# Performance work log

Hardware: AMD Instinct MI355X
Metric: run time of the kernel (lower is better)

## Reference

```python
import jax, jax.numpy as jnp
import numpy as np

T, H, E, I, K = 4096, 2048, 8, 1408, 2


def setup_inputs() -> dict:
    key = jax.random.key(0)
    k1, k2, k3, k4 = jax.random.split(key, 4)
    x = jax.random.normal(k1, (T, H), dtype=jnp.float32)
    router_w = jax.random.normal(k2, (H, E), dtype=jnp.float32) * 0.02
    gate_up_proj = jax.random.normal(k3, (E, H, 2 * I), dtype=jnp.float32) * 0.02
    down_proj = jax.random.normal(k4, (E, I, H), dtype=jnp.float32) * 0.02
    return {"x": x, "router_w": router_w, "gate_up_proj": gate_up_proj, "down_proj": down_proj}


def _moe_forward(x, router_w, gate_up_proj, down_proj):
    # --- Router: softmax over experts, top-k selection (Qwen2-MoE style) ---
    logits = x @ router_w                                  # [T, E]
    probs = jax.nn.softmax(logits, axis=-1)
    topk_w, topk_idx = jax.lax.top_k(probs, K)             # [T, K]

    # --- Permute: replicate tokens per selected expert, stable-sort by expert id ---
    flat_eid = topk_idx.reshape(-1)                        # [T*K]
    rep_x = jnp.repeat(x, K, axis=0)                       # [T*K, H]
    sort_idx = jnp.argsort(flat_eid, stable=True)          # token permute (like ops.permute)
    perm_x = rep_x[sort_idx]                               # [T*K, H] grouped by expert
    perm_eid = flat_eid[sort_idx]                          # [T*K]

    # --- Grouped expert MLP (gate_up GEMM -> SiLU*up -> down GEMM) ---
    # Faithful to grouped-GEMM math; expressed as a fixed loop over E experts
    # with row masking to stay jit-compatible (no data-dependent shapes).
    out = jnp.zeros_like(perm_x)
    for e in range(E):
        gu = perm_x @ gate_up_proj[e]                      # [T*K, 2I]
        gate, up = gu[:, :I], gu[:, I:]
        h = (jax.nn.silu(gate) * up) @ down_proj[e]        # [T*K, H]
        out = out + jnp.where((perm_eid == e)[:, None], h, 0.0)

    # --- Unpermute + weighted combine over top-k ---
    inv_sort = jnp.argsort(sort_idx)                       # inverse permute mapping
    unperm = out[inv_sort].reshape(T, K, H)
    return jnp.einsum('tkh,tk->th', unperm, topk_w)        # [T, H]


def reference(x, router_w, gate_up_proj, down_proj):
    return _moe_forward(x, router_w, gate_up_proj, down_proj)
```

## Files before the change

### kernel.cpp

```cpp
#include <hip/hip_runtime.h>
#include <hip/hip_bf16.h>

#define T_TOK 4096
#define H_DIM 2048
#define E_NUM 8
#define I_DIM 1408
#define RTOT  8192
#define MAXMT 40
#define NT1   11
#define NKT1  64
#define NT2   8
#define NKT2  44

#define QBLK  2080
#define AREG  8320
#define BUFU  16640
#define LDSZ  (4 * BUFU * 2)

typedef __bf16 bf16x8 __attribute__((ext_vector_type(8)));
typedef float  floatx4 __attribute__((ext_vector_type(4)));
typedef unsigned short ushortx8 __attribute__((ext_vector_type(8)));

#define VMCNT(n) asm volatile("s_waitcnt vmcnt(" #n ")" ::: "memory")

__device__ __forceinline__ unsigned short f2bf(float f) {
  union { float f; unsigned u; } v; v.f = f;
  unsigned r = v.u + 0x7FFFu + ((v.u >> 16) & 1u);
  return (unsigned short)(r >> 16);
}

__device__ __forceinline__ void async16(const void* g, void* l) {
  __builtin_amdgcn_global_load_lds(
      (__attribute__((address_space(1))) void*)(g),
      (__attribute__((address_space(3))) void*)(l), 16, 0, 0);
}

__global__ void router_kernel(const float* __restrict__ x, const float* __restrict__ rw,
                              int* __restrict__ topk_idx, float* __restrict__ topk_w,
                              int* __restrict__ counts) {
  int wave = threadIdx.x >> 6, lane = threadIdx.x & 63;
  int t = blockIdx.x * 4 + wave;
  const float* xr = x + (size_t)t * H_DIM;
  float acc[E_NUM];
#pragma unroll
  for (int e = 0; e < E_NUM; e++) acc[e] = 0.f;
  for (int h = lane; h < H_DIM; h += 64) {
    float xv = xr[h];
    const float* wr = rw + h * E_NUM;
#pragma unroll
    for (int e = 0; e < E_NUM; e++) acc[e] += xv * wr[e];
  }
#pragma unroll
  for (int e = 0; e < E_NUM; e++) {
    float v = acc[e];
#pragma unroll
    for (int s = 32; s > 0; s >>= 1) v += __shfl_xor(v, s, 64);
    acc[e] = v;
  }
  if (lane == 0) {
    float mx = acc[0];
#pragma unroll
    for (int e = 1; e < E_NUM; e++) mx = fmaxf(mx, acc[e]);
    float p[E_NUM], s = 0.f;
#pragma unroll
    for (int e = 0; e < E_NUM; e++) { p[e] = __expf(acc[e] - mx); s += p[e]; }
    float inv = 1.0f / s;
    int i0 = 0;
#pragma unroll
    for (int e = 1; e < E_NUM; e++) if (p[e] > p[i0]) i0 = e;
    int i1 = (i0 == 0) ? 1 : 0;
#pragma unroll
    for (int e = 0; e < E_NUM; e++) if (e != i0 && p[e] > p[i1]) i1 = e;
    topk_idx[t * 2]     = i0;
    topk_idx[t * 2 + 1] = i1;
    topk_w[t * 2]       = p[i0] * inv;
    topk_w[t * 2 + 1]   = p[i1] * inv;
    atomicAdd(&counts[i0], 1);
    atomicAdd(&counts[i1], 1);
  }
}

__global__ void scan_kernel(const int* __restrict__ counts, int* __restrict__ cursors,
                            int* __restrict__ tile_e, int* __restrict__ tile_end) {
  if (threadIdx.x == 0) {
    int o = 0, nt = 0;
    for (int e = 0; e < E_NUM; e++) {
      cursors[e] = o;
      int c = counts[e];
      int ntile = (c + 255) >> 8;
      for (int j = 0; j < ntile; j++) { tile_e[nt] = e; tile_end[nt] = o + c; nt++; }
      o += ntile << 8;
    }
    for (; nt < MAXMT; nt++) { tile_e[nt] = -1; tile_end[nt] = 0; }
  }
}

__global__ void assign_kernel(const int* __restrict__ topk_idx, int* __restrict__ cursors,
                              int* __restrict__ row_of, int* __restrict__ tok_of) {
  int i = blockIdx.x * blockDim.x + threadIdx.x;
  int e = topk_idx[i];
  int row = atomicAdd(&cursors[e], 1);
  row_of[i] = row;
  tok_of[row] = i >> 1;
}

__global__ void gather_kernel(const float* __restrict__ x, const int* __restrict__ tok_of,
                              const int* __restrict__ tile_e, const int* __restrict__ tile_end,
                              unsigned short* __restrict__ Xp) {
  int kt = blockIdx.x;
  int mt = blockIdx.y;
  if (tile_e[mt] < 0) return;
  int r = threadIdx.x;
  int row = mt * 256 + r;
  int end = tile_end[mt];
  int rr = row < end ? row : end - 1;
  int tok = tok_of[rr];
  const float4* xr = (const float4*)(x + (size_t)tok * H_DIM + kt * 32);
  float v[32];
#pragma unroll
  for (int p = 0; p < 8; p++) {
    float4 t4 = xr[p];
    v[p * 4 + 0] = t4.x; v[p * 4 + 1] = t4.y; v[p * 4 + 2] = t4.z; v[p * 4 + 3] = t4.w;
  }
  unsigned short* dst = Xp + ((size_t)mt * NKT1 + kt) * 8192;
#pragma unroll
  for (int q = 0; q < 4; q++) {
    ushortx8 o;
#pragma unroll
    for (int j = 0; j < 8; j++) o[j] = f2bf(v[q * 8 + j]);
    *(ushortx8*)(dst + ((size_t)q * 256 + r) * 8) = o;
  }
}

__global__ void convert_gu_kernel(const float* __restrict__ W, unsigned short* __restrict__ W1T) {
  int kt = blockIdx.x;
  int nt = blockIdx.y;
  int e  = blockIdx.z;
  int r  = threadIdx.x;
  int n_phys = nt * 256 + r;
  int b = n_phys >> 4;
  int src_col = ((b >> 1) << 4) + (n_phys & 15) + ((b & 1) ? I_DIM : 0);
  const float* src = W + ((size_t)e * H_DIM + (size_t)kt * 32) * (2 * I_DIM) + src_col;
  float v[32];
#pragma unroll
  for (int k = 0; k < 32; k++) v[k] = src[(size_t)k * (2 * I_DIM)];
  unsigned short* dst = W1T + ((size_t)(e * NT1 + nt) * NKT1 + kt) * 8192;
#pragma unroll
  for (int q = 0; q < 4; q++) {
    ushortx8 o;
#pragma unroll
    for (int j = 0; j < 8; j++) o[j] = f2bf(v[q * 8 + j]);
    *(ushortx8*)(dst + ((size_t)q * 256 + r) * 8) = o;
  }
}

__global__ void convert_dn_kernel(const float* __restrict__ W, unsigned short* __restrict__ WdT) {
  int kt = blockIdx.x;
  int nt = blockIdx.y;
  int e  = blockIdx.z;
  int r  = threadIdx.x;
  int src_col = nt * 256 + r;
  const float* src = W + (size_t)e * I_DIM * H_DIM + (size_t)kt * 32 * H_DIM + src_col;
  float v[32];
#pragma unroll
  for (int k = 0; k < 32; k++) v[k] = src[(size_t)k * H_DIM];
  unsigned short* dst = WdT + ((size_t)(e * NT2 + nt) * NKT2 + kt) * 8192;
#pragma unroll
  for (int q = 0; q < 4; q++) {
    ushortx8 o;
#pragma unroll
    for (int j = 0; j < 8; j++) o[j] = f2bf(v[q * 8 + j]);
    *(ushortx8*)(dst + ((size_t)q * 256 + r) * 8) = o;
  }
}

__global__ __launch_bounds__(512, 2) void gemm1_kernel(
    const unsigned short* __restrict__ Xp, const unsigned short* __restrict__ W1T,
    const int* __restrict__ tile_e, const int* __restrict__ tile_end,
    unsigned short* __restrict__ Hmid) {
  extern __shared__ unsigned short sm[];
  int bid = blockIdx.x;
  int mt = bid % MAXMT, nt = bid / MAXMT;
  int e = tile_e[mt];
  if (e < 0) return;
  int row_end = tile_end[mt];
  int tid = threadIdx.x, wave = tid >> 6, lane = tid & 63;
  int wm = wave >> 2, wn = wave & 3;
  int q = lane >> 4, l15 = lane & 15;

  const unsigned short* gA = Xp  + (size_t)mt * ((size_t)NKT1 * 8192) + tid * 8;
  const unsigned short* gB = W1T + (size_t)(e * NT1 + nt) * ((size_t)NKT1 * 8192) + tid * 8;

  const int u1 = tid + 512;
  const int dA0 = tid * 8 + (tid >> 8) * 32;
  const int dA1 = u1 * 8 + (u1 >> 8) * 32;

  auto STAGE = [&](int buf) {
    unsigned short* sb = sm + buf * BUFU;
    async16(gA,        sb + dA0);
    async16(gA + 4096, sb + dA1);
    async16(gB,        sb + AREG + dA0);
    async16(gB + 4096, sb + AREG + dA1);
    gA += 8192; gB += 8192;
  };

  STAGE(0); STAGE(1);

  const int off_a = q * QBLK + (wm * 128 + l15) * 8;
  const int off_b = AREG + q * QBLK + (wn * 64 + l15) * 8;

  floatx4 acc[8][4] = {};

  for (int t = 0; t < NKT1; t++) {
    if (t + 1 < NKT1) { VMCNT(4); } else { VMCNT(0); }
    __builtin_amdgcn_s_barrier();
    __builtin_amdgcn_sched_barrier(0);
    if (t + 2 < NKT1) STAGE((t + 2) & 3);
    const unsigned short* base = sm + (t & 3) * BUFU;
    bf16x8 a[8], b[4];
#pragma unroll
    for (int mi = 0; mi < 8; mi++) a[mi] = *(const bf16x8*)(base + off_a + mi * 128);
#pragma unroll
    for (int ni = 0; ni < 4; ni++) b[ni] = *(const bf16x8*)(base + off_b + ni * 128);
    __builtin_amdgcn_s_setprio(1);
#pragma unroll
    for (int ni = 0; ni < 4; ni++)
#pragma unroll
      for (int mi = 0; mi < 8; mi++)
        acc[mi][ni] = __builtin_amdgcn_mfma_f32_16x16x32_bf16(a[mi], b[ni], acc[mi][ni], 0, 0, 0);
    __builtin_amdgcn_s_setprio(0);
  }

  const int rt_base = wm * 128 + (lane >> 4) * 4;
  const int lc0 = nt * 128 + wn * 32 + l15;
  unsigned short* Hb = Hmid + (size_t)mt * ((size_t)NKT2 * 8192);
  int rend = row_end - mt * 256;
#pragma unroll
  for (int mi = 0; mi < 8; mi++) {
#pragma unroll
    for (int p = 0; p < 2; p++) {
      int lcol = lc0 + p * 16;
      int kt2 = lcol >> 5, q2 = (lcol >> 3) & 3, j2 = lcol & 7;
      unsigned short* hp = Hb + (size_t)kt2 * 8192 + q2 * 2048 + j2;
#pragma unroll
      for (int r = 0; r < 4; r++) {
        int rt = rt_base + mi * 16 + r;
        if (rt < rend) {
          float g = acc[mi][2 * p][r];
          float u = acc[mi][2 * p + 1][r];
          float s = g / (1.0f + __expf(-g));
          hp[rt * 8] = f2bf(s * u);
        }
      }
    }
  }
}

__global__ __launch_bounds__(512, 2) void gemm2_kernel(
    const unsigned short* __restrict__ Hmid, const unsigned short* __restrict__ WdT,
    const int* __restrict__ tile_e, const int* __restrict__ tile_end,
    float* __restrict__ H2) {
  extern __shared__ unsigned short sm[];
  int bid = blockIdx.x;
  int mt = bid % MAXMT, nt = bid / MAXMT;
  int e = tile_e[mt];
  if (e < 0) return;
  int row_end = tile_end[mt];
  int tid = threadIdx.x, wave = tid >> 6, lane = tid & 63;
  int wm = wave >> 2, wn = wave & 3;
  int q = lane >> 4, l15 = lane & 15;

  const unsigned short* gA = Hmid + (size_t)mt * ((size_t)NKT2 * 8192) + tid * 8;
  const unsigned short* gB = WdT  + (size_t)(e * NT2 + nt) * ((size_t)NKT2 * 8192) + tid * 8;

  const int u1 = tid + 512;
  const int dA0 = tid * 8 + (tid >> 8) * 32;
  const int dA1 = u1 * 8 + (u1 >> 8) * 32;

  auto STAGE = [&](int buf) {
    unsigned short* sb = sm + buf * BUFU;
    async16(gA,        sb + dA0);
    async16(gA + 4096, sb + dA1);
    async16(gB,        sb + AREG + dA0);
    async16(gB + 4096, sb + AREG + dA1);
    gA += 8192; gB += 8192;
  };

  STAGE(0); STAGE(1);

  const int off_a = q * QBLK + (wm * 128 + l15) * 8;
  const int off_b = AREG + q * QBLK + (wn * 64 + l15) * 8;

  floatx4 acc[8][4] = {};

  for (int t = 0; t < NKT2; t++) {
    if (t + 1 < NKT2) { VMCNT(4); } else { VMCNT(0); }
    __builtin_amdgcn_s_barrier();
    __builtin_amdgcn_sched_barrier(0);
    if (t + 2 < NKT2) STAGE(((unsigned)(t + 2)) & 3);
    const unsigned short* base = sm + (t & 3) * BUFU;
    bf16x8 a[8], b[4];
#pragma unroll
    for (int mi = 0; mi < 8; mi++) a[mi] = *(const bf16x8*)(base + off_a + mi * 128);
#pragma unroll
    for (int ni = 0; ni < 4; ni++) b[ni] = *(const bf16x8*)(base + off_b + ni * 128);
    __builtin_amdgcn_s_setprio(1);
#pragma unroll
    for (int ni = 0; ni < 4; ni++)
#pragma unroll
      for (int mi = 0; mi < 8; mi++)
        acc[mi][ni] = __builtin_amdgcn_mfma_f32_16x16x32_bf16(a[mi], b[ni], acc[mi][ni], 0, 0, 0);
    __builtin_amdgcn_s_setprio(0);
  }

  const int rt_base = wm * 128 + (lane >> 4) * 4;
  const int nb = nt * 256 + wn * 64 + l15;
  float* H2b = H2 + (size_t)mt * 256 * H_DIM + nb;
  int rend = row_end - mt * 256;
#pragma unroll
  for (int mi = 0; mi < 8; mi++) {
#pragma unroll
    for (int ni = 0; ni < 4; ni++) {
#pragma unroll
      for (int r = 0; r < 4; r++) {
        int rt = rt_base + mi * 16 + r;
        if (rt < rend) H2b[(size_t)rt * H_DIM + ni * 16] = acc[mi][ni][r];
      }
    }
  }
}

__global__ void combine_kernel(const float* __restrict__ H2, const int* __restrict__ row_of,
                               const float* __restrict__ topk_w, float* __restrict__ out) {
  int t = blockIdx.x >> 1;
  int part = blockIdx.x & 1;
  int c = part * 1024 + threadIdx.x * 4;
  int r0 = row_of[t * 2], r1 = row_of[t * 2 + 1];
  float w0 = topk_w[t * 2], w1 = topk_w[t * 2 + 1];
  float4 a = *(const float4*)(H2 + (size_t)r0 * H_DIM + c);
  float4 b = *(const float4*)(H2 + (size_t)r1 * H_DIM + c);
  float4 o;
  o.x = w0 * a.x + w1 * b.x;
  o.y = w0 * a.y + w1 * b.y;
  o.z = w0 * a.z + w1 * b.z;
  o.w = w0 * a.w + w1 * b.w;
  *(float4*)(out + (size_t)t * H_DIM + c) = o;
}

extern "C" void kernel_launch(void* const* d_in, const int* in_sizes, int n_in,
                              void* d_out, int out_size, void* d_ws, size_t ws_size,
                              hipStream_t stream) {
  const float* x   = (const float*)d_in[0];
  const float* rw  = (const float*)d_in[1];
  const float* wgu = (const float*)d_in[2];
  const float* wdn = (const float*)d_in[3];
  float* out = (float*)d_out;

  static bool attr_done = false;
  if (!attr_done) {
    hipFuncSetAttribute(reinterpret_cast<const void*>(gemm1_kernel),
                        hipFuncAttributeMaxDynamicSharedMemorySize, LDSZ);
    hipFuncSetAttribute(reinterpret_cast<const void*>(gemm2_kernel),
                        hipFuncAttributeMaxDynamicSharedMemorySize, LDSZ);
    attr_done = true;
  }

  char* ws = (char*)d_ws;
  size_t off = 0;
  auto alloc = [&](size_t b) {
    char* p = ws + off;
    off = (off + b + 255) & ~(size_t)255;
    return p;
  };
  unsigned short* W1T  = (unsigned short*)alloc((size_t)E_NUM * NT1 * NKT1 * 8192 * 2);
  unsigned short* WdT  = (unsigned short*)alloc((size_t)E_NUM * NT2 * NKT2 * 8192 * 2);
  unsigned short* Xp   = (unsigned short*)alloc((size_t)MAXMT * NKT1 * 8192 * 2);
  unsigned short* Hmid = (unsigned short*)alloc((size_t)MAXMT * NKT2 * 8192 * 2);
  float* H2            = (float*)alloc((size_t)MAXMT * 256 * H_DIM * 4);
  int*   topk_idx      = (int*)alloc(RTOT * 4);
  float* topk_w        = (float*)alloc(RTOT * 4);
  int*   row_of        = (int*)alloc(RTOT * 4);
  int*   tok_of        = (int*)alloc((size_t)MAXMT * 256 * 4);
  int*   counts        = (int*)alloc(256);
  int*   cursors       = (int*)alloc(256);
  int*   tile_e        = (int*)alloc(64 * 4);
  int*   tile_end      = (int*)alloc(64 * 4);

  hipMemsetAsync(counts, 0, E_NUM * sizeof(int), stream);

  convert_gu_kernel<<<dim3(NKT1, NT1, E_NUM), 256, 0, stream>>>(wgu, W1T);
  convert_dn_kernel<<<dim3(NKT2, NT2, E_NUM), 256, 0, stream>>>(wdn, WdT);
  router_kernel<<<T_TOK / 4, 256, 0, stream>>>(x, rw, topk_idx, topk_w, counts);
  scan_kernel<<<1, 64, 0, stream>>>(counts, cursors, tile_e, tile_end);
  assign_kernel<<<RTOT / 256, 256, 0, stream>>>(topk_idx, cursors, row_of, tok_of);
  gather_kernel<<<dim3(NKT1, MAXMT), 256, 0, stream>>>(x, tok_of, tile_e, tile_end, Xp);
  gemm1_kernel<<<MAXMT * NT1, 512, LDSZ, stream>>>(Xp, W1T, tile_e, tile_end, Hmid);
  gemm2_kernel<<<MAXMT * NT2, 512, LDSZ, stream>>>(Hmid, WdT, tile_e, tile_end, H2);
  combine_kernel<<<T_TOK * 2, 256, 0, stream>>>(H2, row_of, topk_w, out);
}
```

Measured before the change: 741.5 us.

## Row-major bf16 layouts with swizzled LDS, fuse conversions into router and gemm1 launches

Changes the bf16 staging buffers from tiled-packed layouts to plain row-major K-contiguous matrices, and loads them into LDS with an XOR swizzle in place of padding. The gate_up weight conversion now runs in the router launch, and the down weight conversion runs as extra blocks of the gemm1 launch, so the standalone convert kernels disappear. The GEMM main loops split each k-step into two MFMA halves with staggered async loads and barriers, and blocks are remapped per XCD so tiles that share data run on the same die. The intent is fewer launches, better cache locality, and overlap of weight conversion with compute; the cost is more complex synchronization, and gemm1 blocks now compete with conversion blocks for compute units.

```diff
diff --git a/kernel.cpp b/kernel.cpp
--- a/kernel.cpp
+++ b/kernel.cpp
@@ -6,22 +6,26 @@
 #define E_NUM 8
 #define I_DIM 1408
 #define RTOT  8192
+#define N1DIM 2816
 #define MAXMT 40
+#define MAXROWS 10752
 #define NT1   11
 #define NKT1  64
-#define NT2   8
 #define NKT2  44
-
-#define QBLK  2080
-#define AREG  8320
-#define BUFU  16640
-#define LDSZ  (4 * BUFU * 2)
+#define G1_BLOCKS 440
+#define DN_BLOCKS 1408
+#define GU_BLOCKS 5632
+#define RT_BLOCKS 1024
+
+#define BUF1U 16384
+#define LDS1  131072
 
 typedef __bf16 bf16x8 __attribute__((ext_vector_type(8)));
 typedef float  floatx4 __attribute__((ext_vector_type(4)));
 typedef unsigned short ushortx8 __attribute__((ext_vector_type(8)));
 
 #define VMCNT(n) asm volatile("s_waitcnt vmcnt(" #n ")" ::: "memory")
+#define LGK0() do { asm volatile("s_waitcnt lgkmcnt(0)" ::: "memory"); __builtin_amdgcn_sched_barrier(0); } while(0)
 
 __device__ __forceinline__ unsigned short f2bf(float f) {
   union { float f; unsigned u; } v; v.f = f;
@@ -35,63 +39,88 @@
       (__attribute__((address_space(3))) void*)(l), 16, 0, 0);
 }
 
-__global__ void router_kernel(const float* __restrict__ x, const float* __restrict__ rw,
-                              int* __restrict__ topk_idx, float* __restrict__ topk_w,
-                              int* __restrict__ counts) {
-  int wave = threadIdx.x >> 6, lane = threadIdx.x & 63;
-  int t = blockIdx.x * 4 + wave;
-  const float* xr = x + (size_t)t * H_DIM;
-  float acc[E_NUM];
-#pragma unroll
-  for (int e = 0; e < E_NUM; e++) acc[e] = 0.f;
-  for (int h = lane; h < H_DIM; h += 64) {
-    float xv = xr[h];
-    const float* wr = rw + h * E_NUM;
-#pragma unroll
-    for (int e = 0; e < E_NUM; e++) acc[e] += xv * wr[e];
-  }
-#pragma unroll
-  for (int e = 0; e < E_NUM; e++) {
-    float v = acc[e];
-#pragma unroll
-    for (int s = 32; s > 0; s >>= 1) v += __shfl_xor(v, s, 64);
-    acc[e] = v;
-  }
-  if (lane == 0) {
-    float mx = acc[0];
-#pragma unroll
-    for (int e = 1; e < E_NUM; e++) mx = fmaxf(mx, acc[e]);
-    float p[E_NUM], s = 0.f;
-#pragma unroll
-    for (int e = 0; e < E_NUM; e++) { p[e] = __expf(acc[e] - mx); s += p[e]; }
-    float inv = 1.0f / s;
-    int i0 = 0;
-#pragma unroll
-    for (int e = 1; e < E_NUM; e++) if (p[e] > p[i0]) i0 = e;
-    int i1 = (i0 == 0) ? 1 : 0;
-#pragma unroll
-    for (int e = 0; e < E_NUM; e++) if (e != i0 && p[e] > p[i1]) i1 = e;
-    topk_idx[t * 2]     = i0;
-    topk_idx[t * 2 + 1] = i1;
-    topk_w[t * 2]       = p[i0] * inv;
-    topk_w[t * 2 + 1]   = p[i1] * inv;
-    atomicAdd(&counts[i0], 1);
-    atomicAdd(&counts[i1], 1);
+__global__ void gu_router_kernel(const float* __restrict__ W, unsigned short* __restrict__ W1T,
+                                 const float* __restrict__ x, const float* __restrict__ rw,
+                                 int* __restrict__ topk_idx, float* __restrict__ topk_w,
+                                 int* __restrict__ counts) {
+  int bid = blockIdx.x;
+  if (bid < RT_BLOCKS) {
+    int wave = threadIdx.x >> 6, lane = threadIdx.x & 63;
+    int t = bid * 4 + wave;
+    const float* xr = x + (size_t)t * H_DIM;
+    float acc[E_NUM];
+#pragma unroll
+    for (int e = 0; e < E_NUM; e++) acc[e] = 0.f;
+    for (int h = lane; h < H_DIM; h += 64) {
+      float xv = xr[h];
+      const float* wr = rw + h * E_NUM;
+#pragma unroll
+      for (int e = 0; e < E_NUM; e++) acc[e] += xv * wr[e];
+    }
+#pragma unroll
+    for (int e = 0; e < E_NUM; e++) {
+      float v = acc[e];
+#pragma unroll
+      for (int s = 32; s > 0; s >>= 1) v += __shfl_xor(v, s, 64);
+      acc[e] = v;
+    }
+    if (lane == 0) {
+      float mx = acc[0];
+#pragma unroll
+      for (int e = 1; e < E_NUM; e++) mx = fmaxf(mx, acc[e]);
+      float p[E_NUM], s = 0.f;
+#pragma unroll
+      for (int e = 0; e < E_NUM; e++) { p[e] = __expf(acc[e] - mx); s += p[e]; }
+      float inv = 1.0f / s;
+      int i0 = 0;
+#pragma unroll
+      for (int e = 1; e < E_NUM; e++) if (p[e] > p[i0]) i0 = e;
+      int i1 = (i0 == 0) ? 1 : 0;
+#pragma unroll
+      for (int e = 0; e < E_NUM; e++) if (e != i0 && p[e] > p[i1]) i1 = e;
+      topk_idx[t * 2]     = i0;
+      topk_idx[t * 2 + 1] = i1;
+      topk_w[t * 2]       = p[i0] * inv;
+      topk_w[t * 2 + 1]   = p[i1] * inv;
+      atomicAdd(&counts[i0], 1);
+      atomicAdd(&counts[i1], 1);
+    }
+    return;
+  }
+  int b = bid - RT_BLOCKS;
+  int kt = b & 63;
+  int ntb = (b >> 6) % NT1;
+  int e = b / (64 * NT1);
+  int c = threadIdx.x;
+  int n_phys = ntb * 256 + c;
+  int blk = n_phys >> 4;
+  int src_col = ((blk >> 1) << 4) + (n_phys & 15) + ((blk & 1) ? I_DIM : 0);
+  const float* src = W + ((size_t)e * H_DIM + (size_t)kt * 32) * (2 * I_DIM) + src_col;
+  unsigned short* dst = W1T + ((size_t)e * N1DIM + n_phys) * H_DIM + kt * 32;
+  float v[32];
+#pragma unroll
+  for (int k = 0; k < 32; k++) v[k] = src[(size_t)k * (2 * I_DIM)];
+#pragma unroll
+  for (int p = 0; p < 4; p++) {
+    ushortx8 o;
+#pragma unroll
+    for (int j2 = 0; j2 < 8; j2++) o[j2] = f2bf(v[p * 8 + j2]);
+    *(ushortx8*)(dst + p * 8) = o;
   }
 }
 
 __global__ void scan_kernel(const int* __restrict__ counts, int* __restrict__ cursors,
-                            int* __restrict__ tile_e, int* __restrict__ tile_end) {
+                            int* __restrict__ t1e, int* __restrict__ t1m0, int* __restrict__ t1end) {
   if (threadIdx.x == 0) {
-    int o = 0, nt = 0;
+    int o = 0, n1t = 0;
     for (int e = 0; e < E_NUM; e++) {
+      int c = counts[e];
       cursors[e] = o;
-      int c = counts[e];
-      int ntile = (c + 255) >> 8;
-      for (int j = 0; j < ntile; j++) { tile_e[nt] = e; tile_end[nt] = o + c; nt++; }
-      o += ntile << 8;
-    }
-    for (; nt < MAXMT; nt++) { tile_e[nt] = -1; tile_end[nt] = 0; }
+      int n1 = (c + 255) >> 8;
+      for (int j = 0; j < n1; j++) { t1e[n1t] = e; t1m0[n1t] = o + 256 * j; t1end[n1t] = o + c; n1t++; }
+      o += 256 * n1;
+    }
+    for (; n1t < MAXMT; n1t++) t1e[n1t] = -1;
   }
 }
 
@@ -105,151 +134,134 @@
 }
 
 __global__ void gather_kernel(const float* __restrict__ x, const int* __restrict__ tok_of,
-                              const int* __restrict__ tile_e, const int* __restrict__ tile_end,
-                              unsigned short* __restrict__ Xp) {
-  int kt = blockIdx.x;
-  int mt = blockIdx.y;
-  if (tile_e[mt] < 0) return;
-  int r = threadIdx.x;
-  int row = mt * 256 + r;
-  int end = tile_end[mt];
+                              const int* __restrict__ t1e, const int* __restrict__ t1m0,
+                              const int* __restrict__ t1end, unsigned short* __restrict__ Xp) {
+  int mt = blockIdx.x >> 8;
+  if (t1e[mt] < 0) return;
+  int r = blockIdx.x & 255;
+  int row = t1m0[mt] + r;
+  int end = t1end[mt];
   int rr = row < end ? row : end - 1;
   int tok = tok_of[rr];
-  const float4* xr = (const float4*)(x + (size_t)tok * H_DIM + kt * 32);
-  float v[32];
-#pragma unroll
-  for (int p = 0; p < 8; p++) {
-    float4 t4 = xr[p];
-    v[p * 4 + 0] = t4.x; v[p * 4 + 1] = t4.y; v[p * 4 + 2] = t4.z; v[p * 4 + 3] = t4.w;
-  }
-  unsigned short* dst = Xp + ((size_t)mt * NKT1 + kt) * 8192;
-#pragma unroll
-  for (int q = 0; q < 4; q++) {
-    ushortx8 o;
-#pragma unroll
-    for (int j = 0; j < 8; j++) o[j] = f2bf(v[q * 8 + j]);
-    *(ushortx8*)(dst + ((size_t)q * 256 + r) * 8) = o;
-  }
-}
-
-__global__ void convert_gu_kernel(const float* __restrict__ W, unsigned short* __restrict__ W1T) {
-  int kt = blockIdx.x;
-  int nt = blockIdx.y;
-  int e  = blockIdx.z;
-  int r  = threadIdx.x;
-  int n_phys = nt * 256 + r;
-  int b = n_phys >> 4;
-  int src_col = ((b >> 1) << 4) + (n_phys & 15) + ((b & 1) ? I_DIM : 0);
-  const float* src = W + ((size_t)e * H_DIM + (size_t)kt * 32) * (2 * I_DIM) + src_col;
-  float v[32];
-#pragma unroll
-  for (int k = 0; k < 32; k++) v[k] = src[(size_t)k * (2 * I_DIM)];
-  unsigned short* dst = W1T + ((size_t)(e * NT1 + nt) * NKT1 + kt) * 8192;
-#pragma unroll
-  for (int q = 0; q < 4; q++) {
-    ushortx8 o;
-#pragma unroll
-    for (int j = 0; j < 8; j++) o[j] = f2bf(v[q * 8 + j]);
-    *(ushortx8*)(dst + ((size_t)q * 256 + r) * 8) = o;
-  }
-}
-
-__global__ void convert_dn_kernel(const float* __restrict__ W, unsigned short* __restrict__ WdT) {
-  int kt = blockIdx.x;
-  int nt = blockIdx.y;
-  int e  = blockIdx.z;
-  int r  = threadIdx.x;
-  int src_col = nt * 256 + r;
-  const float* src = W + (size_t)e * I_DIM * H_DIM + (size_t)kt * 32 * H_DIM + src_col;
-  float v[32];
-#pragma unroll
-  for (int k = 0; k < 32; k++) v[k] = src[(size_t)k * H_DIM];
-  unsigned short* dst = WdT + ((size_t)(e * NT2 + nt) * NKT2 + kt) * 8192;
-#pragma unroll
-  for (int q = 0; q < 4; q++) {
-    ushortx8 o;
-#pragma unroll
-    for (int j = 0; j < 8; j++) o[j] = f2bf(v[q * 8 + j]);
-    *(ushortx8*)(dst + ((size_t)q * 256 + r) * 8) = o;
-  }
-}
+  const float4* src = (const float4*)(x + (size_t)tok * H_DIM);
+  int i = threadIdx.x;
+  float4 v0 = src[i * 2], v1 = src[i * 2 + 1];
+  ushortx8 o;
+  o[0] = f2bf(v0.x); o[1] = f2bf(v0.y); o[2] = f2bf(v0.z); o[3] = f2bf(v0.w);
+  o[4] = f2bf(v1.x); o[5] = f2bf(v1.y); o[6] = f2bf(v1.z); o[7] = f2bf(v1.w);
+  *(ushortx8*)(Xp + (size_t)row * H_DIM + i * 8) = o;
+}
+
+#define STG_A(lb) do { async16(gA0, (lb) + dA0); gA0 += 32; async16(gA1, (lb) + dA1); gA1 += 32; } while(0)
+#define STG_B(lb) do { async16(gB0, (lb) + dB0); gB0 += 32; async16(gB1, (lb) + dB1); gB1 += 32; } while(0)
 
 __global__ __launch_bounds__(512, 2) void gemm1_kernel(
     const unsigned short* __restrict__ Xp, const unsigned short* __restrict__ W1T,
-    const int* __restrict__ tile_e, const int* __restrict__ tile_end,
+    const float* __restrict__ Wdn, unsigned short* __restrict__ WdT,
+    const int* __restrict__ t1e, const int* __restrict__ t1m0, const int* __restrict__ t1end,
     unsigned short* __restrict__ Hmid) {
   extern __shared__ unsigned short sm[];
   int bid = blockIdx.x;
-  int mt = bid % MAXMT, nt = bid / MAXMT;
-  int e = tile_e[mt];
+  int tid = threadIdx.x;
+  if (bid >= G1_BLOCKS) {
+    int db = bid - G1_BLOCKS;
+    int kt = db % NKT2;
+    int nb = (db / NKT2) & 3;
+    int e  = db / (NKT2 * 4);
+    int n  = nb * 512 + tid;
+    const float* src = Wdn + (size_t)e * I_DIM * H_DIM + (size_t)kt * 32 * H_DIM + n;
+    unsigned short* dst = WdT + ((size_t)e * H_DIM + n) * I_DIM + kt * 32;
+    float v[32];
+#pragma unroll
+    for (int k = 0; k < 32; k++) v[k] = src[(size_t)k * H_DIM];
+#pragma unroll
+    for (int p = 0; p < 4; p++) {
+      ushortx8 o;
+#pragma unroll
+      for (int j2 = 0; j2 < 8; j2++) o[j2] = f2bf(v[p * 8 + j2]);
+      *(ushortx8*)(dst + p * 8) = o;
+    }
+    return;
+  }
+  int xcd = bid & 7, jj = bid >> 3;
+  int mt = xcd * 5 + jj / NT1, nt = jj % NT1;
+  int e = t1e[mt];
   if (e < 0) return;
-  int row_end = tile_end[mt];
-  int tid = threadIdx.x, wave = tid >> 6, lane = tid & 63;
+  int m0 = t1m0[mt], rend = t1end[mt];
+  int n0 = nt * 256;
+  int wave = tid >> 6, lane = tid & 63;
   int wm = wave >> 2, wn = wave & 3;
-  int q = lane >> 4, l15 = lane & 15;
-
-  const unsigned short* gA = Xp  + (size_t)mt * ((size_t)NKT1 * 8192) + tid * 8;
-  const unsigned short* gB = W1T + (size_t)(e * NT1 + nt) * ((size_t)NKT1 * 8192) + tid * 8;
-
-  const int u1 = tid + 512;
-  const int dA0 = tid * 8 + (tid >> 8) * 32;
-  const int dA1 = u1 * 8 + (u1 >> 8) * 32;
-
-  auto STAGE = [&](int buf) {
-    unsigned short* sb = sm + buf * BUFU;
-    async16(gA,        sb + dA0);
-    async16(gA + 4096, sb + dA1);
-    async16(gB,        sb + AREG + dA0);
-    async16(gB + 4096, sb + AREG + dA1);
-    gA += 8192; gB += 8192;
-  };
-
-  STAGE(0); STAGE(1);
-
-  const int off_a = q * QBLK + (wm * 128 + l15) * 8;
-  const int off_b = AREG + q * QBLK + (wn * 64 + l15) * 8;
-
+  int l15 = lane & 15, qq = lane >> 4;
+
+  int u0 = wave * 128 + lane, u1 = u0 + 64;
+  int r0 = u0 >> 2, s0 = (u0 & 3) ^ ((u0 >> 3) & 3);
+  int r1 = u1 >> 2, s1 = (u1 & 3) ^ ((u1 >> 3) & 3);
+  const unsigned short* gA0 = Xp + (size_t)(m0 + r0) * H_DIM + s0 * 8;
+  const unsigned short* gA1 = Xp + (size_t)(m0 + r1) * H_DIM + s1 * 8;
+  const unsigned short* gB0 = W1T + ((size_t)e * N1DIM + (n0 + r0)) * H_DIM + s0 * 8;
+  const unsigned short* gB1 = W1T + ((size_t)e * N1DIM + (n0 + r1)) * H_DIM + s1 * 8;
+  int dA0 = u0 * 8, dA1 = u1 * 8;
+  int dB0 = 8192 + u0 * 8, dB1 = 8192 + u1 * 8;
+
+  int sw = (qq ^ ((l15 >> 1) & 3)) * 16;
+  int sA = (wm * 128 + l15) * 64 + sw;
+  int sB = 16384 + (wn * 64 + l15) * 64 + sw;
+
+  STG_A(sm); STG_B(sm);
+  { unsigned short* lb = sm + BUF1U; STG_A(lb); STG_B(lb); }
   floatx4 acc[8][4] = {};
+  VMCNT(4);
+  __builtin_amdgcn_s_barrier();
 
   for (int t = 0; t < NKT1; t++) {
-    if (t + 1 < NKT1) { VMCNT(4); } else { VMCNT(0); }
-    __builtin_amdgcn_s_barrier();
-    __builtin_amdgcn_sched_barrier(0);
-    if (t + 2 < NKT1) STAGE((t + 2) & 3);
-    const unsigned short* base = sm + (t & 3) * BUFU;
-    bf16x8 a[8], b[4];
-#pragma unroll
-    for (int mi = 0; mi < 8; mi++) a[mi] = *(const bf16x8*)(base + off_a + mi * 128);
-#pragma unroll
-    for (int ni = 0; ni < 4; ni++) b[ni] = *(const bf16x8*)(base + off_b + ni * 128);
+    const char* sb = (const char*)(sm + (t & 3) * BUF1U);
+    unsigned short* lb = sm + ((t + 2) & 3) * BUF1U;
+    bool pf = (t + 2 < NKT1);
+    bf16x8 a[8], b0, b1, b2, b3;
+#pragma unroll
+    for (int fr = 0; fr < 8; fr++) a[fr] = *(const bf16x8*)(sb + sA + fr * 1024);
+    b0 = *(const bf16x8*)(sb + sB);
+    b1 = *(const bf16x8*)(sb + sB + 1024);
+    if (pf) STG_A(lb);
+    __builtin_amdgcn_s_barrier();
+    LGK0();
     __builtin_amdgcn_s_setprio(1);
 #pragma unroll
-    for (int ni = 0; ni < 4; ni++)
-#pragma unroll
-      for (int mi = 0; mi < 8; mi++)
-        acc[mi][ni] = __builtin_amdgcn_mfma_f32_16x16x32_bf16(a[mi], b[ni], acc[mi][ni], 0, 0, 0);
+    for (int fr = 0; fr < 8; fr++) {
+      acc[fr][0] = __builtin_amdgcn_mfma_f32_16x16x32_bf16(a[fr], b0, acc[fr][0], 0, 0, 0);
+      acc[fr][1] = __builtin_amdgcn_mfma_f32_16x16x32_bf16(a[fr], b1, acc[fr][1], 0, 0, 0);
+    }
     __builtin_amdgcn_s_setprio(0);
-  }
-
-  const int rt_base = wm * 128 + (lane >> 4) * 4;
-  const int lc0 = nt * 128 + wn * 32 + l15;
-  unsigned short* Hb = Hmid + (size_t)mt * ((size_t)NKT2 * 8192);
-  int rend = row_end - mt * 256;
-#pragma unroll
-  for (int mi = 0; mi < 8; mi++) {
+    __builtin_amdgcn_s_barrier();
+    b2 = *(const bf16x8*)(sb + sB + 2048);
+    b3 = *(const bf16x8*)(sb + sB + 3072);
+    if (pf) { STG_B(lb); VMCNT(4); } else { VMCNT(0); }
+    __builtin_amdgcn_s_barrier();
+    LGK0();
+    __builtin_amdgcn_s_setprio(1);
+#pragma unroll
+    for (int fr = 0; fr < 8; fr++) {
+      acc[fr][2] = __builtin_amdgcn_mfma_f32_16x16x32_bf16(a[fr], b2, acc[fr][2], 0, 0, 0);
+      acc[fr][3] = __builtin_amdgcn_mfma_f32_16x16x32_bf16(a[fr], b3, acc[fr][3], 0, 0, 0);
+    }
+    __builtin_amdgcn_s_setprio(0);
+  }
+
+  int rb = wm * 128 + (lane >> 4) * 4;
+  int lc0 = nt * 128 + wn * 32 + l15;
+#pragma unroll
+  for (int fr = 0; fr < 8; fr++) {
 #pragma unroll
     for (int p = 0; p < 2; p++) {
       int lcol = lc0 + p * 16;
-      int kt2 = lcol >> 5, q2 = (lcol >> 3) & 3, j2 = lcol & 7;
-      unsigned short* hp = Hb + (size_t)kt2 * 8192 + q2 * 2048 + j2;
 #pragma unroll
       for (int r = 0; r < 4; r++) {
-        int rt = rt_base + mi * 16 + r;
-        if (rt < rend) {
-          float g = acc[mi][2 * p][r];
-          float u = acc[mi][2 * p + 1][r];
+        int arow = m0 + rb + fr * 16 + r;
+        if (arow < rend) {
+          float g = acc[fr][2 * p][r];
+          float u = acc[fr][2 * p + 1][r];
           float s = g / (1.0f + __expf(-g));
-          hp[rt * 8] = f2bf(s * u);
+          Hmid[(size_t)arow * I_DIM + lcol] = f2bf(s * u);
         }
       }
     }
@@ -258,73 +270,84 @@
 
 __global__ __launch_bounds__(512, 2) void gemm2_kernel(
     const unsigned short* __restrict__ Hmid, const unsigned short* __restrict__ WdT,
-    const int* __restrict__ tile_e, const int* __restrict__ tile_end,
+    const int* __restrict__ t1e, const int* __restrict__ t1m0, const int* __restrict__ t1end,
     float* __restrict__ H2) {
   extern __shared__ unsigned short sm[];
   int bid = blockIdx.x;
-  int mt = bid % MAXMT, nt = bid / MAXMT;
-  int e = tile_e[mt];
+  int xcd = bid & 7, jj = bid >> 3;
+  int mt = xcd * 5 + (jj >> 3), nt = jj & 7;
+  int e = t1e[mt];
   if (e < 0) return;
-  int row_end = tile_end[mt];
+  int m0 = t1m0[mt], rend = t1end[mt];
+  int n0 = nt * 256;
   int tid = threadIdx.x, wave = tid >> 6, lane = tid & 63;
   int wm = wave >> 2, wn = wave & 3;
-  int q = lane >> 4, l15 = lane & 15;
-
-  const unsigned short* gA = Hmid + (size_t)mt * ((size_t)NKT2 * 8192) + tid * 8;
-  const unsigned short* gB = WdT  + (size_t)(e * NT2 + nt) * ((size_t)NKT2 * 8192) + tid * 8;
-
-  const int u1 = tid + 512;
-  const int dA0 = tid * 8 + (tid >> 8) * 32;
-  const int dA1 = u1 * 8 + (u1 >> 8) * 32;
-
-  auto STAGE = [&](int buf) {
-    unsigned short* sb = sm + buf * BUFU;
-    async16(gA,        sb + dA0);
-    async16(gA + 4096, sb + dA1);
-    async16(gB,        sb + AREG + dA0);
-    async16(gB + 4096, sb + AREG + dA1);
-    gA += 8192; gB += 8192;
-  };
-
-  STAGE(0); STAGE(1);
-
-  const int off_a = q * QBLK + (wm * 128 + l15) * 8;
-  const int off_b = AREG + q * QBLK + (wn * 64 + l15) * 8;
-
+  int l15 = lane & 15, qq = lane >> 4;
+
+  int u0 = wave * 128 + lane, u1 = u0 + 64;
+  int r0 = u0 >> 2, s0 = (u0 & 3) ^ ((u0 >> 3) & 3);
+  int r1 = u1 >> 2, s1 = (u1 & 3) ^ ((u1 >> 3) & 3);
+  const unsigned short* gA0 = Hmid + (size_t)(m0 + r0) * I_DIM + s0 * 8;
+  const unsigned short* gA1 = Hmid + (size_t)(m0 + r1) * I_DIM + s1 * 8;
+  const unsigned short* gB0 = WdT + ((size_t)e * H_DIM + (n0 + r0)) * I_DIM + s0 * 8;
+  const unsigned short* gB1 = WdT + ((size_t)e * H_DIM + (n0 + r1)) * I_DIM + s1 * 8;
+  int dA0 = u0 * 8, dA1 = u1 * 8;
+  int dB0 = 8192 + u0 * 8, dB1 = 8192 + u1 * 8;
+
+  int sw = (qq ^ ((l15 >> 1) & 3)) * 16;
+  int sA = (wm * 128 + l15) * 64 + sw;
+  int sB = 16384 + (wn * 64 + l15) * 64 + sw;
+
+  STG_A(sm); STG_B(sm);
+  { unsigned short* lb = sm + BUF1U; STG_A(lb); STG_B(lb); }
   floatx4 acc[8][4] = {};
+  VMCNT(4);
+  __builtin_amdgcn_s_barrier();
 
   for (int t = 0; t < NKT2; t++) {
-    if (t + 1 < NKT2) { VMCNT(4); } else { VMCNT(0); }
-    __builtin_amdgcn_s_barrier();
-    __builtin_amdgcn_sched_barrier(0);
-    if (t + 2 < NKT2) STAGE(((unsigned)(t + 2)) & 3);
-    const unsigned short* base = sm + (t & 3) * BUFU;
-    bf16x8 a[8], b[4];
-#pragma unroll
-    for (int mi = 0; mi < 8; mi++) a[mi] = *(const bf16x8*)(base + off_a + mi * 128);
-#pragma unroll
-    for (int ni = 0; ni < 4; ni++) b[ni] = *(const bf16x8*)(base + off_b + ni * 128);
+    const char* sb = (const char*)(sm + (t & 3) * BUF1U);
+    unsigned short* lb = sm + ((t + 2) & 3) * BUF1U;
+    bool pf = (t + 2 < NKT2);
+    bf16x8 a[8], b0, b1, b2, b3;
+#pragma unroll
+    for (int fr = 0; fr < 8; fr++) a[fr] = *(const bf16x8*)(sb + sA + fr * 1024);
+    b0 = *(const bf16x8*)(sb + sB);
+    b1 = *(const bf16x8*)(sb + sB + 1024);
+    if (pf) STG_A(lb);
+    __builtin_amdgcn_s_barrier();
+    LGK0();
     __builtin_amdgcn_s_setprio(1);
 #pragma unroll
-    for (int ni = 0; ni < 4; ni++)
-#pragma unroll
-      for (int mi = 0; mi < 8; mi++)
-        acc[mi][ni] = __builtin_amdgcn_mfma_f32_16x16x32_bf16(a[mi], b[ni], acc[mi][ni], 0, 0, 0);
+    for (int fr = 0; fr < 8; fr++) {
+      acc[fr][0] = __builtin_amdgcn_mfma_f32_16x16x32_bf16(a[fr], b0, acc[fr][0], 0, 0, 0);
+      acc[fr][1] = __builtin_amdgcn_mfma_f32_16x16x32_bf16(a[fr], b1, acc[fr][1], 0, 0, 0);
+    }
     __builtin_amdgcn_s_setprio(0);
-  }
-
-  const int rt_base = wm * 128 + (lane >> 4) * 4;
-  const int nb = nt * 256 + wn * 64 + l15;
-  float* H2b = H2 + (size_t)mt * 256 * H_DIM + nb;
-  int rend = row_end - mt * 256;
-#pragma unroll
-  for (int mi = 0; mi < 8; mi++) {
+    __builtin_amdgcn_s_barrier();
+    b2 = *(const bf16x8*)(sb + sB + 2048);
+    b3 = *(const bf16x8*)(sb + sB + 3072);
+    if (pf) { STG_B(lb); VMCNT(4); } else { VMCNT(0); }
+    __builtin_amdgcn_s_barrier();
+    LGK0();
+    __builtin_amdgcn_s_setprio(1);
+#pragma unroll
+    for (int fr = 0; fr < 8; fr++) {
+      acc[fr][2] = __builtin_amdgcn_mfma_f32_16x16x32_bf16(a[fr], b2, acc[fr][2], 0, 0, 0);
+      acc[fr][3] = __builtin_amdgcn_mfma_f32_16x16x32_bf16(a[fr], b3, acc[fr][3], 0, 0, 0);
+    }
+    __builtin_amdgcn_s_setprio(0);
+  }
+
+  int rb = wm * 128 + (lane >> 4) * 4;
+  int cb = n0 + wn * 64 + l15;
+#pragma unroll
+  for (int fr = 0; fr < 8; fr++) {
 #pragma unroll
     for (int ni = 0; ni < 4; ni++) {
 #pragma unroll
       for (int r = 0; r < 4; r++) {
-        int rt = rt_base + mi * 16 + r;
-        if (rt < rend) H2b[(size_t)rt * H_DIM + ni * 16] = acc[mi][ni][r];
+        int arow = m0 + rb + fr * 16 + r;
+        if (arow < rend) H2[(size_t)arow * H_DIM + cb + ni * 16] = acc[fr][ni][r];
       }
     }
   }
@@ -359,9 +382,9 @@
   static bool attr_done = false;
   if (!attr_done) {
     hipFuncSetAttribute(reinterpret_cast<const void*>(gemm1_kernel),
-                        hipFuncAttributeMaxDynamicSharedMemorySize, LDSZ);
+                        hipFuncAttributeMaxDynamicSharedMemorySize, LDS1);
     hipFuncSetAttribute(reinterpret_cast<const void*>(gemm2_kernel),
-                        hipFuncAttributeMaxDynamicSharedMemorySize, LDSZ);
+                        hipFuncAttributeMaxDynamicSharedMemorySize, LDS1);
     attr_done = true;
   }
 
@@ -372,29 +395,28 @@
     off = (off + b + 255) & ~(size_t)255;
     return p;
   };
-  unsigned short* W1T  = (unsigned short*)alloc((size_t)E_NUM * NT1 * NKT1 * 8192 * 2);
-  unsigned short* WdT  = (unsigned short*)alloc((size_t)E_NUM * NT2 * NKT2 * 8192 * 2);
-  unsigned short* Xp   = (unsigned short*)alloc((size_t)MAXMT * NKT1 * 8192 * 2);
-  unsigned short* Hmid = (unsigned short*)alloc((size_t)MAXMT * NKT2 * 8192 * 2);
-  float* H2            = (float*)alloc((size_t)MAXMT * 256 * H_DIM * 4);
+  unsigned short* W1T  = (unsigned short*)alloc((size_t)E_NUM * N1DIM * H_DIM * 2);
+  unsigned short* WdT  = (unsigned short*)alloc((size_t)E_NUM * H_DIM * I_DIM * 2);
+  unsigned short* Xp   = (unsigned short*)alloc((size_t)MAXROWS * H_DIM * 2);
+  unsigned short* Hmid = (unsigned short*)alloc((size_t)MAXROWS * I_DIM * 2);
+  float* H2            = (float*)alloc((size_t)MAXROWS * H_DIM * 4);
   int*   topk_idx      = (int*)alloc(RTOT * 4);
   float* topk_w        = (float*)alloc(RTOT * 4);
   int*   row_of        = (int*)alloc(RTOT * 4);
-  int*   tok_of        = (int*)alloc((size_t)MAXMT * 256 * 4);
+  int*   tok_of        = (int*)alloc((size_t)MAXROWS * 4);
   int*   counts        = (int*)alloc(256);
   int*   cursors       = (int*)alloc(256);
-  int*   tile_e        = (int*)alloc(64 * 4);
-  int*   tile_end      = (int*)alloc(64 * 4);
+  int*   t1e           = (int*)alloc(MAXMT * 4);
+  int*   t1m0          = (int*)alloc(MAXMT * 4);
+  int*   t1end         = (int*)alloc(MAXMT * 4);
 
   hipMemsetAsync(counts, 0, E_NUM * sizeof(int), stream);
 
-  convert_gu_kernel<<<dim3(NKT1, NT1, E_NUM), 256, 0, stream>>>(wgu, W1T);
-  convert_dn_kernel<<<dim3(NKT2, NT2, E_NUM), 256, 0, stream>>>(wdn, WdT);
-  router_kernel<<<T_TOK / 4, 256, 0, stream>>>(x, rw, topk_idx, topk_w, counts);
-  scan_kernel<<<1, 64, 0, stream>>>(counts, cursors, tile_e, tile_end);
+  gu_router_kernel<<<RT_BLOCKS + GU_BLOCKS, 256, 0, stream>>>(wgu, W1T, x, rw, topk_idx, topk_w, counts);
+  scan_kernel<<<1, 64, 0, stream>>>(counts, cursors, t1e, t1m0, t1end);
   assign_kernel<<<RTOT / 256, 256, 0, stream>>>(topk_idx, cursors, row_of, tok_of);
-  gather_kernel<<<dim3(NKT1, MAXMT), 256, 0, stream>>>(x, tok_of, tile_e, tile_end, Xp);
-  gemm1_kernel<<<MAXMT * NT1, 512, LDSZ, stream>>>(Xp, W1T, tile_e, tile_end, Hmid);
-  gemm2_kernel<<<MAXMT * NT2, 512, LDSZ, stream>>>(Hmid, WdT, tile_e, tile_end, H2);
+  gather_kernel<<<MAXMT * 256, 256, 0, stream>>>(x, tok_of, t1e, t1m0, t1end, Xp);
+  gemm1_kernel<<<G1_BLOCKS + DN_BLOCKS, 512, LDS1, stream>>>(Xp, W1T, wdn, WdT, t1e, t1m0, t1end, Hmid);
+  gemm2_kernel<<<320, 512, LDS1, stream>>>(Hmid, WdT, t1e, t1m0, t1end, H2);
   combine_kernel<<<T_TOK * 2, 256, 0, stream>>>(H2, row_of, topk_w, out);
 }
```

Measured after the change: 709.3 us. 1.05x faster.
